# Performance work log

Measured on AMD Instinct MI355X. Metric: run time of the kernel, lower is better.

## Reference

```python
import jax, jax.numpy as jnp
import numpy as np

N_TP = 4  # number of heterogeneous agent types (experts)


def _mlp(x, w1, b1, w2, b2, w3, b3):
    h = jax.nn.relu(x @ w1 + b1)
    h = jax.nn.relu(h @ w2 + b2)
    return h @ w3 + b3


def setup_inputs() -> dict:
    key = jax.random.key(0)
    ks = jax.random.split(key, 12)
    T, A, D, H, NA = 2048, 128, 64, 64, 16
    s = 0.05
    return {
        "obs": jax.random.normal(ks[0], (T, A, D), dtype=jnp.float32),
        "hete_pick": jax.random.randint(ks[1], (T, A), 0, N_TP, dtype=jnp.int64),
        "gp_sel_summary": jax.random.uniform(ks[2], (T, N_TP), dtype=jnp.float32),
        "W1": jax.random.normal(ks[3], (N_TP, D + N_TP, H), dtype=jnp.float32) * s,
        "b1": jnp.zeros((N_TP, H), jnp.float32),
        "W2": jax.random.normal(ks[4], (N_TP, H, H), dtype=jnp.float32) * s,
        "b2": jnp.zeros((N_TP, H), jnp.float32),
        "W3": jax.random.normal(ks[5], (N_TP, H, NA), dtype=jnp.float32) * s,
        "b3": jnp.zeros((N_TP, NA), jnp.float32),
        "cW1": jax.random.normal(ks[6], (D + N_TP, H), dtype=jnp.float32) * s,
        "cb1": jnp.zeros((H,), jnp.float32),
        "cW2": jax.random.normal(ks[7], (H, H), dtype=jnp.float32) * s,
        "cb2": jnp.zeros((H,), jnp.float32),
        "cW3": jax.random.normal(ks[8], (H, 1), dtype=jnp.float32) * s,
        "cb3": jnp.zeros((1,), jnp.float32),
    }


def reference(obs, hete_pick, gp_sel_summary, W1, b1, W2, b2, W3, b3,
              cW1, cb1, cW2, cb2, cW3, cb3):
    T, A, D = obs.shape
    n_tp = W1.shape[0]
    # hete_info_obs: broadcast group-selection summary over agents, concat to obs
    hete_info = jnp.broadcast_to(gp_sel_summary[:, None, :], (T, A, n_tp))
    x = jnp.concatenate([obs, hete_info.astype(obs.dtype)], axis=-1)  # [T,A,D+n_tp]
    xf = x.reshape(T * A, D + n_tp)
    tp = hete_pick.reshape(T * A)
    # per-type dispatch: mask -> sub-net -> scatter back (expressed as masked select)
    logits = jnp.zeros((T * A, W3.shape[-1]), obs.dtype)
    for t in range(n_tp):
        out_t = _mlp(xf, W1[t], b1[t], W2[t], b2[t], W3[t], b3[t])
        logits = jnp.where((tp == t)[:, None], out_t, logits)
    # central critic runs on all agents
    value = _mlp(xf, cW1, cb1, cW2, cb2, cW3, cb3)  # [T*A,1]
    out = jnp.concatenate([logits, value], axis=-1)  # [T*A, n_action+1]
    return out.reshape(T, A, -1)
```

## Files before the change

### kernel.cpp

```cpp
#include <hip/hip_runtime.h>
#include <stdint.h>


typedef float v4f __attribute__((ext_vector_type(4)));
typedef short v8s __attribute__((ext_vector_type(8)));

#define XS_STR 104
#define HS_STR 136
#define MAXR   176
#define MAXT   11
#define WP2_OFF 30720
#define WP3_OFF 51200

#define SEL4(te, a0, a1, a2, a3) \
    ((te) < 2 ? ((te) == 0 ? (a0) : (a1)) : ((te) == 2 ? (a2) : (a3)))

static __device__ __forceinline__ short f2bf(float f) {
    union { float f; uint32_t u; } c; c.f = f;
    uint32_t u = c.u;
    uint32_t r = (u + 0x7FFFu + ((u >> 16) & 1u)) >> 16;
    return (short)r;
}

__global__ void prep_kernel(const float* __restrict__ W1, const float* __restrict__ cW1,
                            const float* __restrict__ W2, const float* __restrict__ cW2,
                            const float* __restrict__ W3, const float* __restrict__ cW3,
                            short* __restrict__ wp) {
    int b = blockIdx.x, lane = threadIdx.x;
    int nl = lane & 15, quad = lane >> 4;
    short frag[8];
    if (b < 60) {
        int e = b / 12, rem = b % 12, ks = rem / 4, nt = rem % 4;
        int n = nt * 16 + nl;
#pragma unroll
        for (int j = 0; j < 8; j++) {
            int k = ks * 32 + quad * 8 + j;
            float v = 0.f;
            if (k < 68) v = (e < 4) ? W1[(e * 68 + k) * 64 + n] : cW1[k * 64 + n];
            frag[j] = f2bf(v);
        }
    } else if (b < 100) {
        int u = b - 60, e = u / 8, ks = (u % 8) / 4, nt = u % 4;
        int n = nt * 16 + nl;
#pragma unroll
        for (int j = 0; j < 8; j++) {
            int k = ks * 32 + quad * 8 + j;
            frag[j] = f2bf((e < 4) ? W2[(e * 64 + k) * 64 + n] : cW2[k * 64 + n]);
        }
    } else {
        int u = b - 100;
#pragma unroll
        for (int j = 0; j < 8; j++) {
            int ks = (u < 8) ? (u & 1) : (u - 8);
            int k  = ks * 32 + quad * 8 + j;
            float v;
            if (u < 8) { int ee = u >> 1; v = W3[(ee * 64 + k) * 16 + nl]; }
            else       { v = (nl == 0) ? cW3[k] : 0.f; }
            frag[j] = f2bf(v);
        }
    }
    v8s pk = { frag[0], frag[1], frag[2], frag[3], frag[4], frag[5], frag[6], frag[7] };
    *(v8s*)(wp + (size_t)b * 512 + lane * 8) = pk;
}


__global__ __launch_bounds__(256, 3) void main_kernel(
    const float* __restrict__ obs, const int* __restrict__ hete,
    const float* __restrict__ gp, const short* __restrict__ wp,
    const float* __restrict__ b1, const float* __restrict__ b2, const float* __restrict__ b3,
    const float* __restrict__ cb1, const float* __restrict__ cb2, const float* __restrict__ cb3,
    float* __restrict__ out)
{
    __shared__ __align__(16) short buf[MAXR * HS_STR];
    __shared__ int rowtok[MAXR];
    __shared__ int tslot[128];
    __shared__ int wcnt[2][4];

    short* xs = buf;
    short* hs = buf;

    const int b = blockIdx.x;
    const int tid = threadIdx.x, lane = tid & 63, w = tid >> 6;
    const int ml = lane & 15, quad = lane >> 4;
    const int col = w * 16 + ml;
    const size_t base = (size_t)b * 128;

    const int ltk = tid >> 1, hh = tid & 1;
    const float4* src = (const float4*)(obs + (base + ltk) * 64 + hh * 32);
    float4 f[8];
#pragma unroll
    for (int t = 0; t < 8; t++) f[t] = src[t];

    const float* gpb = gp + (size_t)b * 4;
    float g0 = gpb[0], g1 = gpb[1], g2 = gpb[2], g3 = gpb[3];

    if (tid < MAXR) rowtok[tid] = -1;

    int e = 0, rank = 0;
    if (tid < 128) {
        e = hete[base + tid];
        unsigned long long ltm = (1ull << lane) - 1ull;
        unsigned long long m0 = __ballot(e == 0);
        unsigned long long m1 = __ballot(e == 1);
        unsigned long long m2 = __ballot(e == 2);
        unsigned long long m3 = __ballot(e == 3);
        if      (e == 0) rank = __popcll(m0 & ltm);
        else if (e == 1) rank = __popcll(m1 & ltm);
        else if (e == 2) rank = __popcll(m2 & ltm);
        else             rank = __popcll(m3 & ltm);
        if (lane == 0) {
            wcnt[w][0] = __popcll(m0); wcnt[w][1] = __popcll(m1);
            wcnt[w][2] = __popcll(m2); wcnt[w][3] = __popcll(m3);
        }
    }
    __syncthreads();

    int c0 = wcnt[0][0] + wcnt[1][0];
    int c1 = wcnt[0][1] + wcnt[1][1];
    int c2 = wcnt[0][2] + wcnt[1][2];
    int c3 = wcnt[0][3] + wcnt[1][3];
    int p0 = (c0 + 15) & ~15, p1 = (c1 + 15) & ~15;
    int p2 = (c2 + 15) & ~15, p3 = (c3 + 15) & ~15;
    int gs1 = p0, gs2 = p0 + p1, gs3 = p0 + p1 + p2;
    int padded = gs3 + p3;
    int ntiles = padded >> 4;
    int n1 = p1 >> 4, n2 = p2 >> 4, n3 = p3 >> 4;
    int t1 = gs1 >> 4, t2 = gs2 >> 4, t3 = gs3 >> 4;
    int epack = ((0x55555555 & ((1 << (2 * n1)) - 1)) * 1) << (2 * t1)
              | ((0x55555555 & ((1 << (2 * n2)) - 1)) * 2) << (2 * t2)
              | ((0x55555555 & ((1 << (2 * n3)) - 1)) * 3) << (2 * t3);

    if (tid < 128) {
        int gsE  = SEL4(e, 0, gs1, gs2, gs3);
        int woff = (w == 1) ? wcnt[0][e] : 0;
        int slot = gsE + woff + rank;
        rowtok[slot] = tid;
        tslot[tid]   = slot;
    }
    __syncthreads();

    {
        v8s z = { 0, 0, 0, 0, 0, 0, 0, 0 };
        int s = tslot[ltk];
        int rb = s * XS_STR + hh * 32;
#pragma unroll
        for (int t = 0; t < 4; t++) {
            float4 a0 = f[2 * t], a1 = f[2 * t + 1];
            v8s pk = { f2bf(a0.x), f2bf(a0.y), f2bf(a0.z), f2bf(a0.w),
                       f2bf(a1.x), f2bf(a1.y), f2bf(a1.z), f2bf(a1.w) };
            *(v8s*)&xs[rb + t * 8] = pk;
        }
        if (hh) {
            v8s pg = { f2bf(g0), f2bf(g1), f2bf(g2), f2bf(g3), 0, 0, 0, 0 };
            *(v8s*)&xs[s * XS_STR + 64] = pg;
            *(v8s*)&xs[s * XS_STR + 72] = z;
            *(v8s*)&xs[s * XS_STR + 80] = z;
            *(v8s*)&xs[s * XS_STR + 88] = z;
        }
#pragma unroll
        for (int p = 0; p < 2; p++) {
            int r = p * 128 + ltk;
            if (r < padded && rowtok[r] < 0) {
#pragma unroll
                for (int t = 0; t < 4; t++) *(v8s*)&xs[r * XS_STR + hh * 32 + t * 8] = z;
                if (hh) {
                    *(v8s*)&xs[r * XS_STR + 64] = z;
                    *(v8s*)&xs[r * XS_STR + 72] = z;
                    *(v8s*)&xs[r * XS_STR + 80] = z;
                    *(v8s*)&xs[r * XS_STR + 88] = z;
                }
            }
        }
    }
    __syncthreads();

    v4f accE[MAXT], accC[MAXT];
#pragma unroll
    for (int mt = 0; mt < MAXT; mt++) { accE[mt] = (v4f){0,0,0,0}; accC[mt] = (v4f){0,0,0,0}; }

    v8s bC1f[3];
#pragma unroll
    for (int ks = 0; ks < 3; ks++)
        bC1f[ks] = *(const v8s*)(wp + (size_t)((12 + ks) * 4 + w) * 512 + lane * 8);

#pragma unroll
    for (int ks = 0; ks < 3; ks++) {
#pragma unroll
        for (int mt = 0; mt < MAXT; mt++) {
            if (mt < ntiles) {
                int te = (epack >> (2 * mt)) & 3;
                v8s bE = *(const v8s*)(wp + (size_t)((te * 3 + ks) * 4 + w) * 512 + lane * 8);
                v8s a  = *(const v8s*)&xs[(mt * 16 + ml) * XS_STR + ks * 32 + quad * 8];
                accE[mt] = __builtin_amdgcn_mfma_f32_16x16x32_bf16(a, bE,       accE[mt], 0, 0, 0);
                accC[mt] = __builtin_amdgcn_mfma_f32_16x16x32_bf16(a, bC1f[ks], accC[mt], 0, 0, 0);
            }
        }
    }
    __syncthreads();

    {
        float b1e0 = b1[col], b1e1 = b1[64 + col], b1e2 = b1[128 + col], b1e3 = b1[192 + col];
        float cb1v = cb1[col];
#pragma unroll
        for (int mt = 0; mt < MAXT; mt++) {
            if (mt < ntiles) {
                int te = (epack >> (2 * mt)) & 3;
                float bv = SEL4(te, b1e0, b1e1, b1e2, b1e3);
#pragma unroll
                for (int rr = 0; rr < 4; rr++) {
                    int row = mt * 16 + quad * 4 + rr;
                    hs[row * HS_STR + col]      = f2bf(fmaxf(accE[mt][rr] + bv,   0.f));
                    hs[row * HS_STR + 64 + col] = f2bf(fmaxf(accC[mt][rr] + cb1v, 0.f));
                }
            }
        }
    }
    __syncthreads();

    v4f acc2E[MAXT], acc2C[MAXT];
#pragma unroll
    for (int mt = 0; mt < MAXT; mt++) { acc2E[mt] = (v4f){0,0,0,0}; acc2C[mt] = (v4f){0,0,0,0}; }

    v8s bC2f[2];
#pragma unroll
    for (int ks = 0; ks < 2; ks++)
        bC2f[ks] = *(const v8s*)(wp + WP2_OFF + (size_t)((8 + ks) * 4 + w) * 512 + lane * 8);

#pragma unroll
    for (int ks = 0; ks < 2; ks++) {
#pragma unroll
        for (int mt = 0; mt < MAXT; mt++) {
            if (mt < ntiles) {
                int te = (epack >> (2 * mt)) & 3;
                v8s bE = *(const v8s*)(wp + WP2_OFF + (size_t)((te * 2 + ks) * 4 + w) * 512 + lane * 8);
                v8s aE = *(const v8s*)&hs[(mt * 16 + ml) * HS_STR + ks * 32 + quad * 8];
                v8s aC = *(const v8s*)&hs[(mt * 16 + ml) * HS_STR + 64 + ks * 32 + quad * 8];
                acc2E[mt] = __builtin_amdgcn_mfma_f32_16x16x32_bf16(aE, bE,       acc2E[mt], 0, 0, 0);
                acc2C[mt] = __builtin_amdgcn_mfma_f32_16x16x32_bf16(aC, bC2f[ks], acc2C[mt], 0, 0, 0);
            }
        }
    }
    __syncthreads();

    {
        float b2e0 = b2[col], b2e1 = b2[64 + col], b2e2 = b2[128 + col], b2e3 = b2[192 + col];
        float cb2v = cb2[col];
#pragma unroll
        for (int mt = 0; mt < MAXT; mt++) {
            if (mt < ntiles) {
                int te = (epack >> (2 * mt)) & 3;
                float bv = SEL4(te, b2e0, b2e1, b2e2, b2e3);
#pragma unroll
                for (int rr = 0; rr < 4; rr++) {
                    int row = mt * 16 + quad * 4 + rr;
                    hs[row * HS_STR + col]      = f2bf(fmaxf(acc2E[mt][rr] + bv,   0.f));
                    hs[row * HS_STR + 64 + col] = f2bf(fmaxf(acc2C[mt][rr] + cb2v, 0.f));
                }
            }
        }
    }
    __syncthreads();

    v4f accL[3], accV[3];
#pragma unroll
    for (int j = 0; j < 3; j++) { accL[j] = (v4f){0,0,0,0}; accV[j] = (v4f){0,0,0,0}; }

#pragma unroll
    for (int ks = 0; ks < 2; ks++) {
        v8s bV = *(const v8s*)(wp + WP3_OFF + (size_t)(8 + ks) * 512 + lane * 8);
#pragma unroll
        for (int j = 0; j < 3; j++) {
            int mt = w + 4 * j;
            if (mt < ntiles) {
                int te = (epack >> (2 * mt)) & 3;
                v8s bW = *(const v8s*)(wp + WP3_OFF + (size_t)(te * 2 + ks) * 512 + lane * 8);
                v8s aE = *(const v8s*)&hs[(mt * 16 + ml) * HS_STR + ks * 32 + quad * 8];
                v8s aC = *(const v8s*)&hs[(mt * 16 + ml) * HS_STR + 64 + ks * 32 + quad * 8];
                accL[j] = __builtin_amdgcn_mfma_f32_16x16x32_bf16(aE, bW, accL[j], 0, 0, 0);
                accV[j] = __builtin_amdgcn_mfma_f32_16x16x32_bf16(aC, bV, accV[j], 0, 0, 0);
            }
        }
    }

    {
        float b3e0 = b3[ml], b3e1 = b3[16 + ml], b3e2 = b3[32 + ml], b3e3 = b3[48 + ml];
        float cb3v = cb3[0];
#pragma unroll
        for (int j = 0; j < 3; j++) {
            int mt = w + 4 * j;
            if (mt < ntiles) {
                int te = (epack >> (2 * mt)) & 3;
                float bv = SEL4(te, b3e0, b3e1, b3e2, b3e3);
#pragma unroll
                for (int rr = 0; rr < 4; rr++) {
                    int r = mt * 16 + quad * 4 + rr;
                    int tk = rowtok[r];
                    if (tk >= 0) {
                        float* o = out + (base + tk) * 17;
                        o[ml] = accL[j][rr] + bv;
                        if (ml == 0) o[16] = accV[j][rr] + cb3v;
                    }
                }
            }
        }
    }
}


extern "C" void kernel_launch(void* const* d_in, const int* in_sizes, int n_in,
                              void* d_out, int out_size, void* d_ws, size_t ws_size,
                              hipStream_t stream) {
    const float* obs = (const float*)d_in[0];
    const int*  hete = (const int*)d_in[1];
    const float* gp  = (const float*)d_in[2];
    const float* W1  = (const float*)d_in[3];
    const float* b1  = (const float*)d_in[4];
    const float* W2  = (const float*)d_in[5];
    const float* b2  = (const float*)d_in[6];
    const float* W3  = (const float*)d_in[7];
    const float* b3  = (const float*)d_in[8];
    const float* cW1 = (const float*)d_in[9];
    const float* cb1 = (const float*)d_in[10];
    const float* cW2 = (const float*)d_in[11];
    const float* cb2 = (const float*)d_in[12];
    const float* cW3 = (const float*)d_in[13];
    const float* cb3 = (const float*)d_in[14];
    float* out = (float*)d_out;

    short* wp = (short*)d_ws;

    prep_kernel<<<110,  64, 0, stream>>>(W1, cW1, W2, cW2, W3, cW3, wp);
    main_kernel<<<2048, 256, 0, stream>>>(obs, hete, gp, wp,
                                          b1, b2, b3, cb1, cb2, cb3, out);
}
```

Baseline: 165.4 us.

## Pack expert rows contiguously without padding and fix up boundary tiles separately

Rows are grouped by expert without padding each group to 16, so a block always processes exactly 8 tiles instead of up to 11. Each tile takes its expert from the tile's first row, and tiles that straddle an expert boundary get an extra MFMA pass with the next expert's weights, whose results overwrite the rows belonging to that expert. The MFMA operands are swapped so each lane holds 4 consecutive output columns, allowing vectorized bias loads, packed bf16 stores and float4 output writes. Launch bounds are raised to 4 blocks per SM and f2bf uses the native bf16 conversion. The boundary fixups add branches and extra MFMAs, and the higher occupancy target may cause register spills.

```diff
diff --git a/kernel.cpp b/kernel.cpp
--- a/kernel.cpp
+++ b/kernel.cpp
@@ -4,11 +4,10 @@
 
 typedef float v4f __attribute__((ext_vector_type(4)));
 typedef short v8s __attribute__((ext_vector_type(8)));
-
-#define XS_STR 104
+typedef short v4s __attribute__((ext_vector_type(4)));
+typedef float v4fa __attribute__((ext_vector_type(4), aligned(4)));
+
 #define HS_STR 136
-#define MAXR   176
-#define MAXT   11
 #define WP2_OFF 30720
 #define WP3_OFF 51200
 
@@ -16,10 +15,18 @@
     ((te) < 2 ? ((te) == 0 ? (a0) : (a1)) : ((te) == 2 ? (a2) : (a3)))
 
 static __device__ __forceinline__ short f2bf(float f) {
-    union { float f; uint32_t u; } c; c.f = f;
-    uint32_t u = c.u;
-    uint32_t r = (u + 0x7FFFu + ((u >> 16) & 1u)) >> 16;
-    return (short)r;
+    union { __bf16 b; short s; } u;
+    u.b = (__bf16)f;
+    return u.s;
+}
+
+static __device__ __forceinline__ v4s pack4_relu(const v4f a, const v4fa bias) {
+    v4s r;
+    r[0] = f2bf(fmaxf(a[0] + bias[0], 0.f));
+    r[1] = f2bf(fmaxf(a[1] + bias[1], 0.f));
+    r[2] = f2bf(fmaxf(a[2] + bias[2], 0.f));
+    r[3] = f2bf(fmaxf(a[3] + bias[3], 0.f));
+    return r;
 }
 
 __global__ void prep_kernel(const float* __restrict__ W1, const float* __restrict__ cW1,
@@ -64,15 +71,15 @@
 }
 
 
-__global__ __launch_bounds__(256, 3) void main_kernel(
+__global__ __launch_bounds__(256, 4) void main_kernel(
     const float* __restrict__ obs, const int* __restrict__ hete,
     const float* __restrict__ gp, const short* __restrict__ wp,
     const float* __restrict__ b1, const float* __restrict__ b2, const float* __restrict__ b3,
     const float* __restrict__ cb1, const float* __restrict__ cb2, const float* __restrict__ cb3,
     float* __restrict__ out)
 {
-    __shared__ __align__(16) short buf[MAXR * HS_STR];
-    __shared__ int rowtok[MAXR];
+    __shared__ __align__(16) short buf[128 * HS_STR];
+    __shared__ int rowtok[128];
     __shared__ int tslot[128];
     __shared__ int wcnt[2][4];
 
@@ -82,7 +89,6 @@
     const int b = blockIdx.x;
     const int tid = threadIdx.x, lane = tid & 63, w = tid >> 6;
     const int ml = lane & 15, quad = lane >> 4;
-    const int col = w * 16 + ml;
     const size_t base = (size_t)b * 128;
 
     const int ltk = tid >> 1, hh = tid & 1;
@@ -93,8 +99,6 @@
 
     const float* gpb = gp + (size_t)b * 4;
     float g0 = gpb[0], g1 = gpb[1], g2 = gpb[2], g3 = gpb[3];
-
-    if (tid < MAXR) rowtok[tid] = -1;
 
     int e = 0, rank = 0;
     if (tid < 128) {
@@ -115,20 +119,10 @@
     }
     __syncthreads();
 
-    int c0 = wcnt[0][0] + wcnt[1][0];
-    int c1 = wcnt[0][1] + wcnt[1][1];
-    int c2 = wcnt[0][2] + wcnt[1][2];
-    int c3 = wcnt[0][3] + wcnt[1][3];
-    int p0 = (c0 + 15) & ~15, p1 = (c1 + 15) & ~15;
-    int p2 = (c2 + 15) & ~15, p3 = (c3 + 15) & ~15;
-    int gs1 = p0, gs2 = p0 + p1, gs3 = p0 + p1 + p2;
-    int padded = gs3 + p3;
-    int ntiles = padded >> 4;
-    int n1 = p1 >> 4, n2 = p2 >> 4, n3 = p3 >> 4;
-    int t1 = gs1 >> 4, t2 = gs2 >> 4, t3 = gs3 >> 4;
-    int epack = ((0x55555555 & ((1 << (2 * n1)) - 1)) * 1) << (2 * t1)
-              | ((0x55555555 & ((1 << (2 * n2)) - 1)) * 2) << (2 * t2)
-              | ((0x55555555 & ((1 << (2 * n3)) - 1)) * 3) << (2 * t3);
+    const int c0 = wcnt[0][0] + wcnt[1][0];
+    const int c1 = wcnt[0][1] + wcnt[1][1];
+    const int c2 = wcnt[0][2] + wcnt[1][2];
+    const int gs1 = c0, gs2 = c0 + c1, gs3 = c0 + c1 + c2;
 
     if (tid < 128) {
         int gsE  = SEL4(e, 0, gs1, gs2, gs3);
@@ -139,10 +133,14 @@
     }
     __syncthreads();
 
+    int teA[8];
+#pragma unroll
+    for (int mt = 0; mt < 8; mt++)
+        teA[mt] = (mt * 16 >= gs1) + (mt * 16 >= gs2) + (mt * 16 >= gs3);
+
     {
-        v8s z = { 0, 0, 0, 0, 0, 0, 0, 0 };
-        int s = tslot[ltk];
-        int rb = s * XS_STR + hh * 32;
+        int s  = tslot[ltk];
+        int rb = s * HS_STR + hh * 32;
 #pragma unroll
         for (int t = 0; t < 4; t++) {
             float4 a0 = f[2 * t], a1 = f[2 * t + 1];
@@ -152,154 +150,208 @@
         }
         if (hh) {
             v8s pg = { f2bf(g0), f2bf(g1), f2bf(g2), f2bf(g3), 0, 0, 0, 0 };
-            *(v8s*)&xs[s * XS_STR + 64] = pg;
-            *(v8s*)&xs[s * XS_STR + 72] = z;
-            *(v8s*)&xs[s * XS_STR + 80] = z;
-            *(v8s*)&xs[s * XS_STR + 88] = z;
-        }
-#pragma unroll
-        for (int p = 0; p < 2; p++) {
-            int r = p * 128 + ltk;
-            if (r < padded && rowtok[r] < 0) {
-#pragma unroll
-                for (int t = 0; t < 4; t++) *(v8s*)&xs[r * XS_STR + hh * 32 + t * 8] = z;
-                if (hh) {
-                    *(v8s*)&xs[r * XS_STR + 64] = z;
-                    *(v8s*)&xs[r * XS_STR + 72] = z;
-                    *(v8s*)&xs[r * XS_STR + 80] = z;
-                    *(v8s*)&xs[r * XS_STR + 88] = z;
+            v8s z8 = { 0, 0, 0, 0, 0, 0, 0, 0 };
+            *(v8s*)&xs[s * HS_STR + 64] = pg;
+            *(v8s*)&xs[s * HS_STR + 72] = z8;
+            *(v8s*)&xs[s * HS_STR + 80] = z8;
+            *(v8s*)&xs[s * HS_STR + 88] = z8;
+        }
+    }
+    __syncthreads();
+
+    v4f accE[8], accC[8];
+#pragma unroll
+    for (int mt = 0; mt < 8; mt++) { accE[mt] = (v4f){0,0,0,0}; accC[mt] = (v4f){0,0,0,0}; }
+
+    v8s cf1[3];
+#pragma unroll
+    for (int ks = 0; ks < 3; ks++)
+        cf1[ks] = *(const v8s*)(wp + (size_t)((12 + ks) * 4 + w) * 512 + lane * 8);
+
+#pragma unroll
+    for (int ks = 0; ks < 3; ks++) {
+#pragma unroll
+        for (int mt = 0; mt < 8; mt++) {
+            v8s aW = *(const v8s*)(wp + (size_t)((teA[mt] * 3 + ks) * 4 + w) * 512 + lane * 8);
+            v8s xB = *(const v8s*)&xs[(mt * 16 + ml) * HS_STR + ks * 32 + quad * 8];
+            accE[mt] = __builtin_amdgcn_mfma_f32_16x16x32_bf16(aW, xB, accE[mt], 0, 0, 0);
+            accC[mt] = __builtin_amdgcn_mfma_f32_16x16x32_bf16(cf1[ks], xB, accC[mt], 0, 0, 0);
+        }
+    }
+
+    v4f fx[3];
+#pragma unroll
+    for (int bb = 0; bb < 3; bb++) {
+        fx[bb] = (v4f){0,0,0,0};
+        int pos = (bb == 0) ? gs1 : (bb == 1) ? gs2 : gs3;
+        if (pos & 15) {
+            int mtb = pos >> 4, te = bb + 1;
+#pragma unroll
+            for (int ks = 0; ks < 3; ks++) {
+                v8s aW = *(const v8s*)(wp + (size_t)((te * 3 + ks) * 4 + w) * 512 + lane * 8);
+                v8s xB = *(const v8s*)&xs[(mtb * 16 + ml) * HS_STR + ks * 32 + quad * 8];
+                fx[bb] = __builtin_amdgcn_mfma_f32_16x16x32_bf16(aW, xB, fx[bb], 0, 0, 0);
+            }
+        }
+    }
+    __syncthreads();
+
+    {
+        v4fa cbv = *(const v4fa*)(cb1 + w * 16 + quad * 4);
+#pragma unroll
+        for (int mt = 0; mt < 8; mt++) {
+            v4fa bv = *(const v4fa*)(b1 + teA[mt] * 64 + w * 16 + quad * 4);
+            int rb = (mt * 16 + ml) * HS_STR + w * 16 + quad * 4;
+            *(v4s*)&hs[rb]      = pack4_relu(accE[mt], bv);
+            *(v4s*)&hs[rb + 64] = pack4_relu(accC[mt], cbv);
+        }
+#pragma unroll
+        for (int bb = 0; bb < 3; bb++) {
+            int pos = (bb == 0) ? gs1 : (bb == 1) ? gs2 : gs3;
+            if (pos & 15) {
+                int mtb = pos >> 4, te = bb + 1;
+                int row = mtb * 16 + ml;
+                int erow = (row >= gs1) + (row >= gs2) + (row >= gs3);
+                if (erow == te) {
+                    v4fa bv = *(const v4fa*)(b1 + te * 64 + w * 16 + quad * 4);
+                    *(v4s*)&hs[row * HS_STR + w * 16 + quad * 4] = pack4_relu(fx[bb], bv);
                 }
             }
         }
     }
     __syncthreads();
 
-    v4f accE[MAXT], accC[MAXT];
-#pragma unroll
-    for (int mt = 0; mt < MAXT; mt++) { accE[mt] = (v4f){0,0,0,0}; accC[mt] = (v4f){0,0,0,0}; }
-
-    v8s bC1f[3];
-#pragma unroll
-    for (int ks = 0; ks < 3; ks++)
-        bC1f[ks] = *(const v8s*)(wp + (size_t)((12 + ks) * 4 + w) * 512 + lane * 8);
-
-#pragma unroll
-    for (int ks = 0; ks < 3; ks++) {
-#pragma unroll
-        for (int mt = 0; mt < MAXT; mt++) {
-            if (mt < ntiles) {
-                int te = (epack >> (2 * mt)) & 3;
-                v8s bE = *(const v8s*)(wp + (size_t)((te * 3 + ks) * 4 + w) * 512 + lane * 8);
-                v8s a  = *(const v8s*)&xs[(mt * 16 + ml) * XS_STR + ks * 32 + quad * 8];
-                accE[mt] = __builtin_amdgcn_mfma_f32_16x16x32_bf16(a, bE,       accE[mt], 0, 0, 0);
-                accC[mt] = __builtin_amdgcn_mfma_f32_16x16x32_bf16(a, bC1f[ks], accC[mt], 0, 0, 0);
+    v4f acc2E[8], acc2C[8];
+#pragma unroll
+    for (int mt = 0; mt < 8; mt++) { acc2E[mt] = (v4f){0,0,0,0}; acc2C[mt] = (v4f){0,0,0,0}; }
+
+    v8s cf2[2];
+#pragma unroll
+    for (int ks = 0; ks < 2; ks++)
+        cf2[ks] = *(const v8s*)(wp + WP2_OFF + (size_t)((8 + ks) * 4 + w) * 512 + lane * 8);
+
+#pragma unroll
+    for (int ks = 0; ks < 2; ks++) {
+#pragma unroll
+        for (int mt = 0; mt < 8; mt++) {
+            v8s aW = *(const v8s*)(wp + WP2_OFF + (size_t)((teA[mt] * 2 + ks) * 4 + w) * 512 + lane * 8);
+            v8s hE = *(const v8s*)&hs[(mt * 16 + ml) * HS_STR + ks * 32 + quad * 8];
+            v8s hC = *(const v8s*)&hs[(mt * 16 + ml) * HS_STR + 64 + ks * 32 + quad * 8];
+            acc2E[mt] = __builtin_amdgcn_mfma_f32_16x16x32_bf16(aW, hE, acc2E[mt], 0, 0, 0);
+            acc2C[mt] = __builtin_amdgcn_mfma_f32_16x16x32_bf16(cf2[ks], hC, acc2C[mt], 0, 0, 0);
+        }
+    }
+
+    v4f fx2[3];
+#pragma unroll
+    for (int bb = 0; bb < 3; bb++) {
+        fx2[bb] = (v4f){0,0,0,0};
+        int pos = (bb == 0) ? gs1 : (bb == 1) ? gs2 : gs3;
+        if (pos & 15) {
+            int mtb = pos >> 4, te = bb + 1;
+#pragma unroll
+            for (int ks = 0; ks < 2; ks++) {
+                v8s aW = *(const v8s*)(wp + WP2_OFF + (size_t)((te * 2 + ks) * 4 + w) * 512 + lane * 8);
+                v8s hE = *(const v8s*)&hs[(mtb * 16 + ml) * HS_STR + ks * 32 + quad * 8];
+                fx2[bb] = __builtin_amdgcn_mfma_f32_16x16x32_bf16(aW, hE, fx2[bb], 0, 0, 0);
             }
         }
     }
     __syncthreads();
 
     {
-        float b1e0 = b1[col], b1e1 = b1[64 + col], b1e2 = b1[128 + col], b1e3 = b1[192 + col];
-        float cb1v = cb1[col];
-#pragma unroll
-        for (int mt = 0; mt < MAXT; mt++) {
-            if (mt < ntiles) {
-                int te = (epack >> (2 * mt)) & 3;
-                float bv = SEL4(te, b1e0, b1e1, b1e2, b1e3);
-#pragma unroll
-                for (int rr = 0; rr < 4; rr++) {
-                    int row = mt * 16 + quad * 4 + rr;
-                    hs[row * HS_STR + col]      = f2bf(fmaxf(accE[mt][rr] + bv,   0.f));
-                    hs[row * HS_STR + 64 + col] = f2bf(fmaxf(accC[mt][rr] + cb1v, 0.f));
+        v4fa cbv = *(const v4fa*)(cb2 + w * 16 + quad * 4);
+#pragma unroll
+        for (int mt = 0; mt < 8; mt++) {
+            v4fa bv = *(const v4fa*)(b2 + teA[mt] * 64 + w * 16 + quad * 4);
+            int rb = (mt * 16 + ml) * HS_STR + w * 16 + quad * 4;
+            *(v4s*)&hs[rb]      = pack4_relu(acc2E[mt], bv);
+            *(v4s*)&hs[rb + 64] = pack4_relu(acc2C[mt], cbv);
+        }
+#pragma unroll
+        for (int bb = 0; bb < 3; bb++) {
+            int pos = (bb == 0) ? gs1 : (bb == 1) ? gs2 : gs3;
+            if (pos & 15) {
+                int mtb = pos >> 4, te = bb + 1;
+                int row = mtb * 16 + ml;
+                int erow = (row >= gs1) + (row >= gs2) + (row >= gs3);
+                if (erow == te) {
+                    v4fa bv = *(const v4fa*)(b2 + te * 64 + w * 16 + quad * 4);
+                    *(v4s*)&hs[row * HS_STR + w * 16 + quad * 4] = pack4_relu(fx2[bb], bv);
                 }
             }
         }
     }
     __syncthreads();
 
-    v4f acc2E[MAXT], acc2C[MAXT];
-#pragma unroll
-    for (int mt = 0; mt < MAXT; mt++) { acc2E[mt] = (v4f){0,0,0,0}; acc2C[mt] = (v4f){0,0,0,0}; }
-
-    v8s bC2f[2];
-#pragma unroll
-    for (int ks = 0; ks < 2; ks++)
-        bC2f[ks] = *(const v8s*)(wp + WP2_OFF + (size_t)((8 + ks) * 4 + w) * 512 + lane * 8);
+    v4f accL[2], accV[2];
+#pragma unroll
+    for (int j = 0; j < 2; j++) { accL[j] = (v4f){0,0,0,0}; accV[j] = (v4f){0,0,0,0}; }
 
 #pragma unroll
     for (int ks = 0; ks < 2; ks++) {
-#pragma unroll
-        for (int mt = 0; mt < MAXT; mt++) {
-            if (mt < ntiles) {
-                int te = (epack >> (2 * mt)) & 3;
-                v8s bE = *(const v8s*)(wp + WP2_OFF + (size_t)((te * 2 + ks) * 4 + w) * 512 + lane * 8);
-                v8s aE = *(const v8s*)&hs[(mt * 16 + ml) * HS_STR + ks * 32 + quad * 8];
-                v8s aC = *(const v8s*)&hs[(mt * 16 + ml) * HS_STR + 64 + ks * 32 + quad * 8];
-                acc2E[mt] = __builtin_amdgcn_mfma_f32_16x16x32_bf16(aE, bE,       acc2E[mt], 0, 0, 0);
-                acc2C[mt] = __builtin_amdgcn_mfma_f32_16x16x32_bf16(aC, bC2f[ks], acc2C[mt], 0, 0, 0);
-            }
-        }
-    }
-    __syncthreads();
+        v8s aV = *(const v8s*)(wp + WP3_OFF + (size_t)(8 + ks) * 512 + lane * 8);
+#pragma unroll
+        for (int j = 0; j < 2; j++) {
+            int mt = w + 4 * j;
+            int te = (mt * 16 >= gs1) + (mt * 16 >= gs2) + (mt * 16 >= gs3);
+            v8s aW = *(const v8s*)(wp + WP3_OFF + (size_t)(te * 2 + ks) * 512 + lane * 8);
+            v8s hE = *(const v8s*)&hs[(mt * 16 + ml) * HS_STR + ks * 32 + quad * 8];
+            v8s hC = *(const v8s*)&hs[(mt * 16 + ml) * HS_STR + 64 + ks * 32 + quad * 8];
+            accL[j] = __builtin_amdgcn_mfma_f32_16x16x32_bf16(aW, hE, accL[j], 0, 0, 0);
+            accV[j] = __builtin_amdgcn_mfma_f32_16x16x32_bf16(aV, hC, accV[j], 0, 0, 0);
+        }
+    }
+
+    v4f fxL[3];
+#pragma unroll
+    for (int bb = 0; bb < 3; bb++) {
+        fxL[bb] = (v4f){0,0,0,0};
+        int pos = (bb == 0) ? gs1 : (bb == 1) ? gs2 : gs3;
+        int mtb = pos >> 4;
+        if ((pos & 15) && (mtb & 3) == w) {
+            int te = bb + 1;
+#pragma unroll
+            for (int ks = 0; ks < 2; ks++) {
+                v8s aW = *(const v8s*)(wp + WP3_OFF + (size_t)(te * 2 + ks) * 512 + lane * 8);
+                v8s hE = *(const v8s*)&hs[(mtb * 16 + ml) * HS_STR + ks * 32 + quad * 8];
+                fxL[bb] = __builtin_amdgcn_mfma_f32_16x16x32_bf16(aW, hE, fxL[bb], 0, 0, 0);
+            }
+        }
+    }
 
     {
-        float b2e0 = b2[col], b2e1 = b2[64 + col], b2e2 = b2[128 + col], b2e3 = b2[192 + col];
-        float cb2v = cb2[col];
-#pragma unroll
-        for (int mt = 0; mt < MAXT; mt++) {
-            if (mt < ntiles) {
-                int te = (epack >> (2 * mt)) & 3;
-                float bv = SEL4(te, b2e0, b2e1, b2e2, b2e3);
-#pragma unroll
-                for (int rr = 0; rr < 4; rr++) {
-                    int row = mt * 16 + quad * 4 + rr;
-                    hs[row * HS_STR + col]      = f2bf(fmaxf(acc2E[mt][rr] + bv,   0.f));
-                    hs[row * HS_STR + 64 + col] = f2bf(fmaxf(acc2C[mt][rr] + cb2v, 0.f));
-                }
-            }
-        }
-    }
-    __syncthreads();
-
-    v4f accL[3], accV[3];
-#pragma unroll
-    for (int j = 0; j < 3; j++) { accL[j] = (v4f){0,0,0,0}; accV[j] = (v4f){0,0,0,0}; }
-
-#pragma unroll
-    for (int ks = 0; ks < 2; ks++) {
-        v8s bV = *(const v8s*)(wp + WP3_OFF + (size_t)(8 + ks) * 512 + lane * 8);
-#pragma unroll
-        for (int j = 0; j < 3; j++) {
+        float cb3v = cb3[0];
+#pragma unroll
+        for (int j = 0; j < 2; j++) {
             int mt = w + 4 * j;
-            if (mt < ntiles) {
-                int te = (epack >> (2 * mt)) & 3;
-                v8s bW = *(const v8s*)(wp + WP3_OFF + (size_t)(te * 2 + ks) * 512 + lane * 8);
-                v8s aE = *(const v8s*)&hs[(mt * 16 + ml) * HS_STR + ks * 32 + quad * 8];
-                v8s aC = *(const v8s*)&hs[(mt * 16 + ml) * HS_STR + 64 + ks * 32 + quad * 8];
-                accL[j] = __builtin_amdgcn_mfma_f32_16x16x32_bf16(aE, bW, accL[j], 0, 0, 0);
-                accV[j] = __builtin_amdgcn_mfma_f32_16x16x32_bf16(aC, bV, accV[j], 0, 0, 0);
-            }
-        }
-    }
-
-    {
-        float b3e0 = b3[ml], b3e1 = b3[16 + ml], b3e2 = b3[32 + ml], b3e3 = b3[48 + ml];
-        float cb3v = cb3[0];
-#pragma unroll
-        for (int j = 0; j < 3; j++) {
-            int mt = w + 4 * j;
-            if (mt < ntiles) {
-                int te = (epack >> (2 * mt)) & 3;
-                float bv = SEL4(te, b3e0, b3e1, b3e2, b3e3);
-#pragma unroll
-                for (int rr = 0; rr < 4; rr++) {
-                    int r = mt * 16 + quad * 4 + rr;
-                    int tk = rowtok[r];
-                    if (tk >= 0) {
-                        float* o = out + (base + tk) * 17;
-                        o[ml] = accL[j][rr] + bv;
-                        if (ml == 0) o[16] = accV[j][rr] + cb3v;
-                    }
+            int te = (mt * 16 >= gs1) + (mt * 16 >= gs2) + (mt * 16 >= gs3);
+            int row = mt * 16 + ml;
+            int erow = (row >= gs1) + (row >= gs2) + (row >= gs3);
+            int tk = rowtok[row];
+            float* o = out + (base + (size_t)tk) * 17;
+            if (erow == te) {
+                v4fa b3v = *(const v4fa*)(b3 + te * 16 + quad * 4);
+                v4fa ov = { accL[j][0] + b3v[0], accL[j][1] + b3v[1],
+                            accL[j][2] + b3v[2], accL[j][3] + b3v[3] };
+                *(v4fa*)(o + quad * 4) = ov;
+            }
+            if (quad == 0) o[16] = accV[j][0] + cb3v;
+        }
+#pragma unroll
+        for (int bb = 0; bb < 3; bb++) {
+            int pos = (bb == 0) ? gs1 : (bb == 1) ? gs2 : gs3;
+            int mtb = pos >> 4;
+            if ((pos & 15) && (mtb & 3) == w) {
+                int row = mtb * 16 + ml;
+                int erow = (row >= gs1) + (row >= gs2) + (row >= gs3);
+                if (erow == bb + 1) {
+                    v4fa b3v = *(const v4fa*)(b3 + (bb + 1) * 16 + quad * 4);
+                    int tk = rowtok[row];
+                    float* o = out + (base + (size_t)tk) * 17;
+                    v4fa ov = { fxL[bb][0] + b3v[0], fxL[bb][1] + b3v[1],
+                                fxL[bb][2] + b3v[2], fxL[bb][3] + b3v[3] };
+                    *(v4fa*)(o + quad * 4) = ov;
                 }
             }
         }
```

Result: faster. 158.1 us (-4.4%).
